# Kernel optimization log

Hardware: AMD Instinct MI355X
Metric: run time of the kernel (lower is better)

## Reference

```python
import jax, jax.numpy as jnp
import numpy as np

# --- config constants (GaussianSceneGridCreatorConfig / GaussianPointMatcherConfig) ---
CONF_LEVEL = 0.95
CHI2_95_DF3 = 7.8147279  # chi-square 0.95 quantile, 3 dof -> confidence ellipsoid scale
VOXEL_SIZE_FACTOR = 3.0
MAX_GRID = 1024
OVERSIZED_THRESH = 64
CLIP_Q = 0.01
PAD_FACTOR = 0.1
LOG_2PI = 1.8378770664093453


def quat_to_rotmat(q):
    # q: [G,4] (w,x,y,z), normalized inside
    q = q / jnp.linalg.norm(q, axis=-1, keepdims=True)
    w, x, y, z = q[:, 0], q[:, 1], q[:, 2], q[:, 3]
    R = jnp.stack([
        1 - 2 * (y * y + z * z), 2 * (x * y - w * z), 2 * (x * z + w * y),
        2 * (x * y + w * z), 1 - 2 * (x * x + z * z), 2 * (y * z - w * x),
        2 * (x * z - w * y), 2 * (y * z + w * x), 1 - 2 * (x * x + y * y),
    ], axis=-1).reshape(-1, 3, 3)
    return R


def setup_inputs() -> dict:
    key = jax.random.key(0)
    k1, k2, k3, k4 = jax.random.split(key, 4)
    G, P = 2048, 16384
    positions = jax.random.uniform(k1, (G, 3), dtype=jnp.float32) * 100.0
    scales = jax.random.uniform(k2, (G, 3), dtype=jnp.float32) * 0.4 + 0.02
    quaternions = jax.random.normal(k3, (G, 4), dtype=jnp.float32)
    points = jax.random.uniform(k4, (P, 3), dtype=jnp.float32) * 100.0
    return {"positions": positions, "scales": scales, "quaternions": quaternions,
            "points": points, "K": 8}


def reference(positions, scales, quaternions, points, K):
    # ---- per-sphere AABB at confidence level (gaussian_scene_aabb) ----
    R = quat_to_rotmat(quaternions)                     # [G,3,3]
    s2 = scales * scales                                # [G,3]
    diag_cov = jnp.einsum('gij,gj->gi', R * R, s2)      # diag of R S S^T R^T
    k = jnp.sqrt(jnp.float32(CHI2_95_DF3))
    radius = k * jnp.sqrt(diag_cov)                     # [G,3] per-axis half extents
    min_c = positions - radius
    max_c = positions + radius

    # ---- robust global scene AABB (quantile clip + padding) ----
    lo = jnp.quantile(min_c, CLIP_Q, axis=0)
    hi = jnp.quantile(max_c, 1.0 - CLIP_Q, axis=0)
    size = hi - lo
    gmin = lo - PAD_FACTOR * size                       # scene_min_offset, [3]

    # ---- voxel size from median radius ----
    voxel_size = jnp.median(radius[:, 0]) * VOXEL_SIZE_FACTOR

    # ---- sparse grid insertion (insert_gaussian_sphere_kernel), as membership test ----
    grid_min = jnp.clip(jnp.floor((min_c - gmin) / voxel_size).astype(jnp.int32), 0, MAX_GRID - 1)
    grid_max = jnp.clip(jnp.floor((max_c - gmin) / voxel_size).astype(jnp.int32), 0, MAX_GRID - 1)
    extent = grid_max - grid_min + 1
    num_vox = extent[:, 0].astype(jnp.int64) * extent[:, 1].astype(jnp.int64) * extent[:, 2].astype(jnp.int64)
    oversized = num_vox > OVERSIZED_THRESH              # [G] always-checked spheres

    pv = jnp.floor((points - gmin) / voxel_size).astype(jnp.int32)  # point voxel cells [P,3]
    # candidate mask [P,G]: point's cell lies inside the sphere's inserted AABB, or oversized
    in_box = ((pv[:, 0:1] >= grid_min[None, :, 0]) & (pv[:, 0:1] <= grid_max[None, :, 0]) &
              (pv[:, 1:2] >= grid_min[None, :, 1]) & (pv[:, 1:2] <= grid_max[None, :, 1]) &
              (pv[:, 2:3] >= grid_min[None, :, 2]) & (pv[:, 2:3] <= grid_max[None, :, 2]))
    mask = in_box | oversized[None, :]                  # [P,G]

    # ---- per-sphere precompute: covariance inverse + log normalization factor ----
    cov_inv = jnp.einsum('gij,gj,gkj->gik', R, 1.0 / s2, R)            # [G,3,3]
    log_norm = -1.5 * LOG_2PI - jnp.sum(jnp.log(scales), axis=-1)       # [G]

    # ---- quadratic form (p-c)^T Sinv (p-c) via expansion, avoiding [P,G,3] ----
    b = jnp.einsum('gij,gj->gi', cov_inv, positions)                    # [G,3]
    c0 = jnp.einsum('gi,gi->g', b, positions)                           # [G]
    pp = (points[:, :, None] * points[:, None, :]).reshape(-1, 9)       # [P,9]
    quad = pp @ cov_inv.reshape(-1, 9).T - 2.0 * (points @ b.T) + c0[None, :]  # [P,G]
    logp = log_norm[None, :] - 0.5 * quad                               # [P,G]

    # ---- top-K spheres per point over grid candidates ----
    score = jnp.where(mask, logp, -jnp.inf)
    vals, idx = jax.lax.top_k(score, K)                                 # [P,K]
    finite = jnp.isfinite(vals)
    probs = jnp.where(finite, jnp.exp(jnp.where(finite, vals, 0.0)), 0.0)
    topk_ids = jnp.where(finite, idx, -1).astype(jnp.int32)
    return topk_ids, probs
```

## Files before the change

### kernel.cpp

```cpp
#include <hip/hip_runtime.h>
#include <math.h>

#pragma clang fp contract(off)

#define G_N 2048
#define P_N 16384
#define K_TOP 8
#define NBUCK 32768
#define BCAP 128

#define GUARD64 ((1ull << 20) | (1ull << 41) | (1ull << 62))

#define OFF_CNT 16
#define OFF_OVC (OFF_CNT + NBUCK)
#define OFF_OVL (OFF_OVC + 1)
#define OFF_ENT (OFF_OVL + G_N)
#define OFF_BOX (OFF_ENT + NBUCK * BCAP)

__device__ __forceinline__ void quat_R(const float* quat, int g, float R[3][3]) {
    float q0 = quat[g * 4 + 0], q1 = quat[g * 4 + 1], q2 = quat[g * 4 + 2], q3 = quat[g * 4 + 3];
    float nrm = sqrtf(q0 * q0 + q1 * q1 + q2 * q2 + q3 * q3);
    float w = q0 / nrm, x = q1 / nrm, y = q2 / nrm, z = q3 / nrm;
    R[0][0] = 1.0f - 2.0f * (y * y + z * z);
    R[0][1] = 2.0f * (x * y - w * z);
    R[0][2] = 2.0f * (x * z + w * y);
    R[1][0] = 2.0f * (x * y + w * z);
    R[1][1] = 1.0f - 2.0f * (x * x + z * z);
    R[1][2] = 2.0f * (y * z - w * x);
    R[2][0] = 2.0f * (x * z - w * y);
    R[2][1] = 2.0f * (y * z + w * x);
    R[2][2] = 1.0f - 2.0f * (x * x + y * y);
}

__device__ __forceinline__ float radius_axis(const float R[3][3], float s2x, float s2y, float s2z, int a) {
    float dc = (R[a][0] * R[a][0]) * s2x + (R[a][1] * R[a][1]) * s2y + (R[a][2] * R[a][2]) * s2z;
    return sqrtf(7.8147279f) * sqrtf(dc);
}

__device__ __forceinline__ void grid_params(const float* ws, float gmn[3], float& vox) {
#pragma unroll
    for (int t = 0; t < 3; ++t) {
        float lo = ws[t], hi = ws[3 + t];
        float size = hi - lo;
        gmn[t] = lo - 0.1f * size;
    }
    vox = ws[6] * 3.0f;
}

__device__ __forceinline__ float score_g(const float* __restrict__ pos, const float* __restrict__ scl,
                                         const float* __restrict__ quat, int g,
                                         float px, float py, float pz,
                                         float pp0, float pp1, float pp2,
                                         float pp4, float pp5, float pp8) {
    float R[3][3];
    quat_R(quat, g, R);
    float sx = scl[g * 3 + 0], sy = scl[g * 3 + 1], sz = scl[g * 3 + 2];
    float inv2x = 1.0f / (sx * sx), inv2y = 1.0f / (sy * sy), inv2z = 1.0f / (sz * sz);
    float C[3][3];
#pragma unroll
    for (int i = 0; i < 3; ++i) {
        float t0 = R[i][0] * inv2x, t1 = R[i][1] * inv2y, t2 = R[i][2] * inv2z;
#pragma unroll
        for (int k = 0; k < 3; ++k)
            C[i][k] = t0 * R[k][0] + t1 * R[k][1] + t2 * R[k][2];
    }
    float gx = pos[g * 3 + 0], gy = pos[g * 3 + 1], gz = pos[g * 3 + 2];
    float b0 = C[0][0] * gx + C[0][1] * gy + C[0][2] * gz;
    float b1 = C[1][0] * gx + C[1][1] * gy + C[1][2] * gz;
    float b2 = C[2][0] * gx + C[2][1] * gy + C[2][2] * gz;
    float c0 = b0 * gx + b1 * gy + b2 * gz;
    float log_norm = -2.7568155996140179f - (logf(sx) + logf(sy) + logf(sz));
    float s1 = pp0 * C[0][0];
    s1 = fmaf(pp1, C[0][1], s1);
    s1 = fmaf(pp2, C[0][2], s1);
    s1 = fmaf(pp1, C[1][0], s1);
    s1 = fmaf(pp4, C[1][1], s1);
    s1 = fmaf(pp5, C[1][2], s1);
    s1 = fmaf(pp2, C[2][0], s1);
    s1 = fmaf(pp5, C[2][1], s1);
    s1 = fmaf(pp8, C[2][2], s1);
    float d = px * b0;
    d = fmaf(py, b1, d);
    d = fmaf(pz, b2, d);
    float quad = fmaf(-2.0f, d, s1) + c0;
    return fmaf(-0.5f, quad, log_norm);
}

__global__ __launch_bounds__(1024) void k_stats(const float* __restrict__ pos,
                                                const float* __restrict__ scl,
                                                const float* __restrict__ quat,
                                                float* __restrict__ ws) {
    int which = blockIdx.x;
    int tid = threadIdx.x;
    if (which == 7) {
        unsigned* u = (unsigned*)ws;
        for (int i = tid; i < NBUCK; i += 1024) u[OFF_CNT + i] = 0u;
        if (tid == 0) u[OFF_OVC] = 0u;
        return;
    }
    __shared__ float buf[G_N];
    int a = (which < 3) ? which : (which < 6 ? which - 3 : 0);
    for (int g = tid; g < G_N; g += 1024) {
        float R[3][3];
        quat_R(quat, g, R);
        float sx = scl[g * 3 + 0], sy = scl[g * 3 + 1], sz = scl[g * 3 + 2];
        float rad = radius_axis(R, sx * sx, sy * sy, sz * sz, a);
        float v;
        if (which < 3)      v = pos[g * 3 + a] - rad;
        else if (which < 6) v = pos[g * 3 + a] + rad;
        else                v = rad;
        buf[g] = v;
    }
    __syncthreads();
    for (int k = 2; k <= G_N; k <<= 1) {
        for (int j = k >> 1; j > 0; j >>= 1) {
            for (int i = tid; i < G_N; i += 1024) {
                int partner = i ^ j;
                if (partner > i) {
                    bool up = ((i & k) == 0);
                    float va = buf[i], vb = buf[partner];
                    if ((va > vb) == up) { buf[i] = vb; buf[partner] = va; }
                }
            }
            __syncthreads();
        }
    }
    if (tid == 0) {
        float qq;
        if (which < 3) qq = 0.01f * 2047.0f;
        else if (which < 6) qq = 0.99f * 2047.0f;
        else qq = 0.5f * 2047.0f;
        int lo = (int)floorf(qq);
        float fr = qq - (float)lo;
        ws[which] = buf[lo] * (1.0f - fr) + buf[lo + 1] * fr;
    }
}

__global__ __launch_bounds__(256) void k_build(const float* __restrict__ pos,
                                               const float* __restrict__ scl,
                                               const float* __restrict__ quat,
                                               float* __restrict__ ws) {
    int g = blockIdx.x * blockDim.x + threadIdx.x;
    if (g >= G_N) return;
    float gmn[3], vox;
    grid_params(ws, gmn, vox);

    float R[3][3];
    quat_R(quat, g, R);
    float sx = scl[g * 3 + 0], sy = scl[g * 3 + 1], sz = scl[g * 3 + 2];
    float s2x = sx * sx, s2y = sy * sy, s2z = sz * sz;
    int gmini[3], gmaxi[3];
    long long nv = 1;
#pragma unroll
    for (int t = 0; t < 3; ++t) {
        float rad = radius_axis(R, s2x, s2y, s2z, t);
        float p = pos[g * 3 + t];
        int lo = (int)floorf(((p - rad) - gmn[t]) / vox);
        int hi = (int)floorf(((p + rad) - gmn[t]) / vox);
        lo = lo < 0 ? 0 : (lo > 1023 ? 1023 : lo);
        hi = hi < 0 ? 0 : (hi > 1023 ? 1023 : hi);
        gmini[t] = lo; gmaxi[t] = hi;
        nv *= (long long)(hi - lo + 1);
    }
    unsigned* u = (unsigned*)ws;
    bool oversized = nv > 64;
    if (oversized) {
        unsigned slot = atomicAdd(&u[OFF_OVC], 1u);
        u[OFF_OVL + slot] = (unsigned)g;
        gmini[0] = gmini[1] = gmini[2] = 0;
        gmaxi[0] = gmaxi[1] = gmaxi[2] = 2047;
    } else {
        for (int z = gmini[2]; z <= gmaxi[2]; ++z)
            for (int y = gmini[1]; y <= gmaxi[1]; ++y)
                for (int x = gmini[0]; x <= gmaxi[0]; ++x) {
                    unsigned h = ((unsigned)x * 73856093u ^ (unsigned)y * 19349663u
                                ^ (unsigned)z * 83492791u) & (NBUCK - 1);
                    unsigned old = atomicAdd(&u[OFF_CNT + h], 1u);
                    if (old < BCAP) u[OFF_ENT + h * BCAP + old] = (unsigned)g;
                }
    }
    unsigned long long A = (unsigned long long)gmini[0]
                         | ((unsigned long long)gmini[1] << 21)
                         | ((unsigned long long)gmini[2] << 42);
    unsigned long long B = ((unsigned long long)gmaxi[0]
                         | ((unsigned long long)gmaxi[1] << 21)
                         | ((unsigned long long)gmaxi[2] << 42)) | GUARD64;
    uint4* bx = (uint4*)(u + OFF_BOX);
    bx[g] = make_uint4((unsigned)(A & 0xffffffffu), (unsigned)(A >> 32),
                       (unsigned)(B & 0xffffffffu), (unsigned)(B >> 32));
}

__device__ __forceinline__ void ins8(float tv[K_TOP], int ti[K_TOP], float sc, int id) {
    bool dup = false;
#pragma unroll
    for (int j = 0; j < K_TOP; ++j) dup |= (ti[j] == id);
    if (dup) return;
    bool better = (sc > tv[K_TOP - 1]) || (sc == tv[K_TOP - 1] && id < ti[K_TOP - 1]);
    if (!better) return;
    tv[K_TOP - 1] = sc;
    ti[K_TOP - 1] = id;
#pragma unroll
    for (int j = K_TOP - 1; j > 0; --j) {
        bool sw = (tv[j] > tv[j - 1]) || (tv[j] == tv[j - 1] && ti[j] < ti[j - 1]);
        if (sw) {
            float fv = tv[j]; tv[j] = tv[j - 1]; tv[j - 1] = fv;
            int iv = ti[j]; ti[j] = ti[j - 1]; ti[j - 1] = iv;
        }
    }
}

__global__ __launch_bounds__(64) void k_match(const float* __restrict__ pos,
                                              const float* __restrict__ scl,
                                              const float* __restrict__ quat,
                                              const float* __restrict__ pts,
                                              const float* __restrict__ ws,
                                              float* __restrict__ out) {
    int p = blockIdx.x * 64 + threadIdx.x;
    float gmn[3], vox;
    grid_params(ws, gmn, vox);
    float px = pts[p * 3 + 0], py = pts[p * 3 + 1], pz = pts[p * 3 + 2];
    float fpx = floorf((px - gmn[0]) / vox);
    float fpy = floorf((py - gmn[1]) / vox);
    float fpz = floorf((pz - gmn[2]) / vox);
    bool valid = (fpx >= 0.0f) & (fpx <= 1023.0f) & (fpy >= 0.0f) & (fpy <= 1023.0f)
               & (fpz >= 0.0f) & (fpz <= 1023.0f);

    float pp0 = px * px, pp1 = px * py, pp2 = px * pz;
    float pp4 = py * py, pp5 = py * pz, pp8 = pz * pz;

    float tv[K_TOP];
    int ti[K_TOP];
#pragma unroll
    for (int j = 0; j < K_TOP; ++j) { tv[j] = -INFINITY; ti[j] = 0x7fffffff; }

    const unsigned* u = (const unsigned*)ws;
    const uint4* bx = (const uint4*)(u + OFF_BOX);

    if (valid) {
        int vx = (int)fpx, vy = (int)fpy, vz = (int)fpz;
        unsigned long long PV = (unsigned long long)(unsigned)vx
                              | ((unsigned long long)(unsigned)vy << 21)
                              | ((unsigned long long)(unsigned)vz << 42);
        unsigned long long PVG = PV | GUARD64;
        unsigned h = ((unsigned)vx * 73856093u ^ (unsigned)vy * 19349663u
                    ^ (unsigned)vz * 83492791u) & (NBUCK - 1);
        unsigned cnt = u[OFF_CNT + h];
        if (cnt <= BCAP) {
            for (unsigned i = 0; i < cnt; ++i) {
                int g = (int)u[OFF_ENT + h * BCAP + i];
                uint4 b4 = bx[g];
                unsigned long long A = (unsigned long long)b4.x | ((unsigned long long)b4.y << 32);
                unsigned long long B = (unsigned long long)b4.z | ((unsigned long long)b4.w << 32);
                if ((((PVG - A) & (B - PV)) & GUARD64) == GUARD64) {
                    float sc = score_g(pos, scl, quat, g, px, py, pz, pp0, pp1, pp2, pp4, pp5, pp8);
                    ins8(tv, ti, sc, g);
                }
            }
        } else {
            for (int g = 0; g < G_N; ++g) {
                uint4 b4 = bx[g];
                unsigned long long A = (unsigned long long)b4.x | ((unsigned long long)b4.y << 32);
                unsigned long long B = (unsigned long long)b4.z | ((unsigned long long)b4.w << 32);
                if ((((PVG - A) & (B - PV)) & GUARD64) == GUARD64) {
                    float sc = score_g(pos, scl, quat, g, px, py, pz, pp0, pp1, pp2, pp4, pp5, pp8);
                    ins8(tv, ti, sc, g);
                }
            }
        }
    }
    unsigned ovc = u[OFF_OVC];
    for (unsigned i = 0; i < ovc; ++i) {
        int g = (int)u[OFF_OVL + i];
        float sc = score_g(pos, scl, quat, g, px, py, pz, pp0, pp1, pp2, pp4, pp5, pp8);
        ins8(tv, ti, sc, g);
    }

#pragma unroll
    for (int j = 0; j < K_TOP; ++j) {
        bool fin = tv[j] > -INFINITY;
        out[p * K_TOP + j] = fin ? (float)ti[j] : -1.0f;
        out[P_N * K_TOP + p * K_TOP + j] = fin ? expf(tv[j]) : 0.0f;
    }
}

extern "C" void kernel_launch(void* const* d_in, const int* in_sizes, int n_in,
                              void* d_out, int out_size, void* d_ws, size_t ws_size,
                              hipStream_t stream) {
    const float* pos = (const float*)d_in[0];
    const float* scl = (const float*)d_in[1];
    const float* quat = (const float*)d_in[2];
    const float* pts = (const float*)d_in[3];
    float* ws = (float*)d_ws;
    float* out = (float*)d_out;

    k_stats<<<dim3(8), dim3(1024), 0, stream>>>(pos, scl, quat, ws);
    k_build<<<dim3(G_N / 256), dim3(256), 0, stream>>>(pos, scl, quat, ws);
    k_match<<<dim3(P_N / 64), dim3(64), 0, stream>>>(pos, scl, quat, pts, ws, out);
}
```

Before: 105.0 us.

## Replace bitonic sort with radix select for quantile statistics

The quantile/median stats kernel no longer sorts all 2048 values with a shared-memory bitonic sort. It finds the needed order statistics with a 4-pass 8-bit radix select over order-preserving uint keys, then uses one extra atomic pass to get the next element for interpolation. This cuts the dozens of barrier-separated sort stages down to a few passes, at the cost of shared-memory atomic contention and serial histogram scans done by a single thread.

```diff
diff --git a/kernel.cpp b/kernel.cpp
--- a/kernel.cpp
+++ b/kernel.cpp
@@ -86,6 +86,15 @@
     return fmaf(-0.5f, quad, log_norm);
 }
 
+__device__ __forceinline__ unsigned f2ord(float f) {
+    unsigned u = __float_as_uint(f);
+    return (u & 0x80000000u) ? ~u : (u | 0x80000000u);
+}
+__device__ __forceinline__ float ord2f(unsigned u) {
+    unsigned v = (u & 0x80000000u) ? (u ^ 0x80000000u) : ~u;
+    return __uint_as_float(v);
+}
+
 __global__ __launch_bounds__(1024) void k_stats(const float* __restrict__ pos,
                                                 const float* __restrict__ scl,
                                                 const float* __restrict__ quat,
@@ -98,9 +107,11 @@
         if (tid == 0) u[OFF_OVC] = 0u;
         return;
     }
-    __shared__ float buf[G_N];
     int a = (which < 3) ? which : (which < 6 ? which - 3 : 0);
-    for (int g = tid; g < G_N; g += 1024) {
+    unsigned keys[2];
+#pragma unroll
+    for (int i = 0; i < 2; ++i) {
+        int g = tid + i * 1024;
         float R[3][3];
         quat_R(quat, g, R);
         float sx = scl[g * 3 + 0], sy = scl[g * 3 + 1], sz = scl[g * 3 + 2];
@@ -109,30 +120,63 @@
         if (which < 3)      v = pos[g * 3 + a] - rad;
         else if (which < 6) v = pos[g * 3 + a] + rad;
         else                v = rad;
-        buf[g] = v;
-    }
+        keys[i] = f2ord(v);
+    }
+
+    __shared__ unsigned hist[256];
+    __shared__ unsigned sel[2];
+    __shared__ unsigned res2[2];
+
+    int rank0 = (which < 3) ? 20 : ((which < 6) ? 2026 : 1023);
+    unsigned prefix = 0, pmask = 0, rank = (unsigned)rank0;
+#pragma unroll
+    for (int pass = 0; pass < 4; ++pass) {
+        int shift = 24 - 8 * pass;
+        if (tid < 256) hist[tid] = 0u;
+        __syncthreads();
+#pragma unroll
+        for (int i = 0; i < 2; ++i) {
+            unsigned k = keys[i];
+            if ((k & pmask) == prefix) atomicAdd(&hist[(k >> shift) & 255u], 1u);
+        }
+        __syncthreads();
+        if (tid == 0) {
+            unsigned cum = 0;
+            unsigned d = 0;
+            for (; d < 256; ++d) {
+                unsigned c = hist[d];
+                if (cum + c > rank) break;
+                cum += c;
+            }
+            sel[0] = d;
+            sel[1] = rank - cum;
+        }
+        __syncthreads();
+        prefix |= sel[0] << shift;
+        pmask |= 0xFFu << shift;
+        rank = sel[1];
+        __syncthreads();
+    }
+    if (tid < 2) res2[tid] = (tid == 0) ? 0u : 0xFFFFFFFFu;
     __syncthreads();
-    for (int k = 2; k <= G_N; k <<= 1) {
-        for (int j = k >> 1; j > 0; j >>= 1) {
-            for (int i = tid; i < G_N; i += 1024) {
-                int partner = i ^ j;
-                if (partner > i) {
-                    bool up = ((i & k) == 0);
-                    float va = buf[i], vb = buf[partner];
-                    if ((va > vb) == up) { buf[i] = vb; buf[partner] = va; }
-                }
-            }
-            __syncthreads();
-        }
-    }
+#pragma unroll
+    for (int i = 0; i < 2; ++i) {
+        unsigned k = keys[i];
+        if (k <= prefix) atomicAdd(&res2[0], 1u);
+        else atomicMin(&res2[1], k);
+    }
+    __syncthreads();
     if (tid == 0) {
+        unsigned vlo = prefix;
+        unsigned vhi = (res2[0] >= (unsigned)(rank0 + 2)) ? prefix : res2[1];
+        float flo = ord2f(vlo), fhi = ord2f(vhi);
         float qq;
         if (which < 3) qq = 0.01f * 2047.0f;
         else if (which < 6) qq = 0.99f * 2047.0f;
         else qq = 0.5f * 2047.0f;
         int lo = (int)floorf(qq);
         float fr = qq - (float)lo;
-        ws[which] = buf[lo] * (1.0f - fr) + buf[lo + 1] * fr;
+        ws[which] = flo * (1.0f - fr) + fhi * fr;
     }
 }
 
```

New measurement: 125.0 us. +19.1%, slower.
